# Optimization experiments

Hardware: AMD Instinct MI355X
Metric: run time of the kernel (lower is better)

## Reference

```python
import jax, jax.numpy as jnp
import numpy as np

S = 32        # num_subdomains
D = 1         # in_size
WIDTH = 128   # width_size
DEPTH = 4     # eqx MLP depth -> 1 input layer + (DEPTH-1) hidden layers + 1 output layer
N = 262144    # collocation points
TOL = 1e-8


def setup_inputs() -> dict:
    key = jax.random.key(0)
    ks = jax.random.split(key, 7)
    # subdomain i = [(i-0.5)/S, (i+1.5)/S] -> center (i+0.5)/S, half-width 1/S
    centers = ((jnp.arange(S, dtype=jnp.float32) + 0.5) / S)[:, None]          # (S, D)
    scales = jnp.full((S, D), 1.0 / S, dtype=jnp.float32)                       # (S, D)

    def unif(k, shape, fan_in):  # equinox Linear init: U(-1/sqrt(fan_in), 1/sqrt(fan_in))
        lim = 1.0 / np.sqrt(fan_in)
        return jax.random.uniform(k, shape, jnp.float32, -lim, lim)

    W_in = unif(ks[0], (S, WIDTH, D), D)
    b_in = unif(ks[1], (S, WIDTH), D)
    W_hid = unif(ks[2], (S, DEPTH - 1, WIDTH, WIDTH), WIDTH)
    b_hid = unif(ks[3], (S, DEPTH - 1, WIDTH), WIDTH)
    W_out = unif(ks[4], (S, 1, WIDTH), WIDTH)
    b_out = unif(ks[5], (S, 1), WIDTH)
    x = jax.random.uniform(ks[6], (N, D), jnp.float32, 0.0, 1.0)
    return {"x": x, "W_in": W_in, "b_in": b_in, "W_hid": W_hid, "b_hid": b_hid,
            "W_out": W_out, "b_out": b_out, "centers": centers, "scales": scales}


def reference(x, W_in, b_in, W_hid, b_hid, W_out, b_out, centers, scales):
    # normalized coords per subdomain: (S, n, D)
    u = (x[None, :, :] - centers[:, None, :]) / scales[:, None, :]
    # partition-of-unity cosine window, product over dims, normalized over subdomains
    raw = jnp.prod(jnp.where(jnp.abs(u) < 1.0, jnp.cos(0.5 * jnp.pi * u) ** 2, 0.0), axis=-1)  # (S, n)
    w = raw / (jnp.sum(raw, axis=0, keepdims=True) + TOL)                                       # (S, n)

    def body(total, p):
        Wi, bi, Wh, bh, Wo, bo, xn, wk = p
        h = jnp.tanh(xn @ Wi.T + bi)                      # (n, WIDTH)
        for l in range(DEPTH - 1):                        # static unroll over hidden layers
            h = jnp.tanh(h @ Wh[l].T + bh[l])
        out = (h @ Wo.T + bo)[:, 0]                       # (n,)
        return total + wk * out, None

    total, _ = jax.lax.scan(body, jnp.zeros(x.shape[0], x.dtype),
                            (W_in, b_in, W_hid, b_hid, W_out, b_out, u, w))
    # ansatz = identity
    return total
```

## Files before the change

### kernel.cpp

```cpp
#include <hip/hip_runtime.h>

#define NS 32
#define WID 128
#define NHID 3
#define NPTS 262144
#define PTILE 256
#define TMLP 512
#define TPB 68

#define TASKS_OFF 512
#define WF_OFF (TASKS_OFF + 2 * NPTS * 4)
#define TANH_C 2.8853900817779268f

typedef _Float16 f16x2 __attribute__((ext_vector_type(2)));
typedef _Float16 f16x4 __attribute__((ext_vector_type(4)));
typedef _Float16 f16x8 __attribute__((ext_vector_type(8)));
typedef __fp16 fp16x2 __attribute__((ext_vector_type(2)));
typedef float f32x4 __attribute__((ext_vector_type(4)));

union U4H8 { uint4 u; f16x8 h; };
union PK2 { fp16x2 p; f16x2 h; };

__device__ __forceinline__ f16x2 pk2(float a, float b) {
    PK2 u; u.p = __builtin_amdgcn_cvt_pkrtz(a, b); return u.h;
}

__device__ __forceinline__ float tanh_fast(float v) {
    float a = v * TANH_C;
    float e; asm("v_exp_f32 %0, %1" : "=v"(e) : "v"(a));
    float d = e + 1.0f;
    float r; asm("v_rcp_f32 %0, %1" : "=v"(r) : "v"(d));
    return fmaf(-2.0f, r, 1.0f);
}

__device__ __forceinline__ float tanh_pre(float a) {
    float e; asm("v_exp_f32 %0, %1" : "=v"(e) : "v"(a));
    float d = e + 1.0f;
    float r; asm("v_rcp_f32 %0, %1" : "=v"(r) : "v"(d));
    return fmaf(-2.0f, r, 1.0f);
}

__device__ __forceinline__ float coswin(float u) {
    if (fabsf(u) >= 1.0f) return 0.0f;
    float rev = u * 0.25f;
    float c; asm("v_cos_f32 %0, %1" : "=v"(c) : "v"(rev));
    return c * c;
}


__global__ void k_count(const float* __restrict__ x, int* __restrict__ counts, int n) {
    __shared__ int loc[NS];
    int t = threadIdx.x;
    if (t < NS) loc[t] = 0;
    __syncthreads();
    int i = blockIdx.x * blockDim.x + t;
    if (i < n) {
        float tt = x[i] * 32.0f;
        int j = (int)floorf(tt); j = min(max(j, 0), 31);
        atomicAdd(&loc[j], 1);
        float u = tt - (float)j - 0.5f;
        int nb = (u > 0.0f) ? j + 1 : j - 1;
        if (u != 0.0f && nb >= 0 && nb < NS) atomicAdd(&loc[nb], 1);
    }
    __syncthreads();
    if (t < NS) atomicAdd(&counts[t], loc[t]);
}

__global__ void k_scan(const int* __restrict__ counts, int* __restrict__ offsets,
                       int* __restrict__ cursors) {
    if (threadIdx.x == 0) {
        int acc = 0;
        for (int s = 0; s < NS; ++s) { offsets[s] = acc; cursors[s] = acc; acc += counts[s]; }
    }
}

__global__ void k_scatter(const float* __restrict__ x, int* __restrict__ cursors,
                          int* __restrict__ tasks, int n) {
    __shared__ int loc[NS];
    __shared__ int base[NS];
    int t = threadIdx.x;
    if (t < NS) loc[t] = 0;
    __syncthreads();
    int i = blockIdx.x * blockDim.x + t;
    int j = -1, nb = -1, sj = 0, snb = 0;
    if (i < n) {
        float tt = x[i] * 32.0f;
        j = min(max((int)floorf(tt), 0), 31);
        sj = atomicAdd(&loc[j], 1);
        float u = tt - (float)j - 0.5f;
        int nb2 = (u > 0.0f) ? j + 1 : j - 1;
        if (u != 0.0f && nb2 >= 0 && nb2 < NS) { nb = nb2; snb = atomicAdd(&loc[nb], 1); }
    }
    __syncthreads();
    if (t < NS) base[t] = atomicAdd(&cursors[t], loc[t]);
    __syncthreads();
    if (i < n) {
        tasks[base[j] + sj] = i;
        if (nb >= 0) tasks[base[nb] + snb] = i;
    }
}


__global__ void k_prepw(const float* __restrict__ Wh, uint4* __restrict__ WfU4) {
    int tid = blockIdx.x * blockDim.x + threadIdx.x;
    if (tid >= 32 * 3 * 8 * 4 * 64) return;
    int lane = tid & 63;
    int s    = (tid >> 6) & 3;
    int t8   = (tid >> 8) & 7;
    int v    = tid >> 11;
    int o    = 16 * t8 + (lane & 15);
    const float* src = Wh + ((size_t)v * 128 + o) * 128;
    unsigned short b[8];
#pragma unroll
    for (int e = 0; e < 8; ++e) {
        int k = 32 * s + 4 * (lane >> 4) + (e & 3) + 16 * (e >> 2);
        _Float16 hv = (_Float16)(src[k] * TANH_C);
        b[e] = *(unsigned short*)&hv;
    }
    uint4 outv;
    outv.x = (unsigned)b[0] | ((unsigned)b[1] << 16);
    outv.y = (unsigned)b[2] | ((unsigned)b[3] << 16);
    outv.z = (unsigned)b[4] | ((unsigned)b[5] << 16);
    outv.w = (unsigned)b[6] | ((unsigned)b[7] << 16);
    WfU4[((size_t)(v * 8 + t8) * 4 + s) * 64 + lane] = outv;
}


__global__ __launch_bounds__(TMLP, 4) void k_mlp(
    const float* __restrict__ x, const float* __restrict__ W_in, const float* __restrict__ b_in,
    const float* __restrict__ b_hid, const float* __restrict__ W_out, const float* __restrict__ b_out,
    const float* __restrict__ centers, const float* __restrict__ scales,
    const int* __restrict__ counts, const int* __restrict__ offsets, const int* __restrict__ tasks,
    const uint4* __restrict__ WfU4, float* __restrict__ out) {

    const int bin = blockIdx.y;
    const int tile = blockIdx.x;
    const int cnt = counts[bin];
    if (tile * PTILE >= cnt) return;
    const int start = offsets[bin];

    __shared__ __align__(256) _Float16 HT[8][4096];
    __shared__ float lU[PTILE], lWgt[PTILE];
    __shared__ int lTid[PTILE];

    const int t = threadIdx.x;
    const int lane = t & 63;
    const int l15 = t & 15;
    const int g = (t >> 4) & 3;
    const int w = t >> 6;

    if (t < PTILE) {
        int idx = tile * PTILE + t;
        if (idx < cnt) {
            int pid = tasks[start + idx];
            lTid[t] = pid;
            float xx = x[pid];
            float u = (xx - centers[bin]) * (1.0f / scales[bin]);
            lU[t] = u;
            float rs = coswin(u);
            int other = bin + (u > 0.0f ? 1 : -1);
            float ro = 0.0f;
            if (other >= 0 && other < NS)
                ro = coswin((xx - centers[other]) * (1.0f / scales[other]));
            lWgt[t] = rs / (rs + ro + 1e-8f);
        } else { lTid[t] = -1; lU[t] = 0.0f; lWgt[t] = 0.0f; }
    }
    __syncthreads();

    {
        float4 ua = *(const float4*)&lU[w * 32 + 4 * g];
        float4 ub = *(const float4*)&lU[w * 32 + 16 + 4 * g];
        const float* Win = W_in + bin * WID;
        const float* Bi  = b_in + bin * WID;
#pragma unroll
        for (int t8 = 0; t8 < 8; ++t8) {
            int o = 16 * t8 + l15;
            float wv = Win[o], bv = Bi[o];
            f16x2 h00 = pk2(tanh_fast(fmaf(ua.x, wv, bv)), tanh_fast(fmaf(ua.y, wv, bv)));
            f16x2 h01 = pk2(tanh_fast(fmaf(ua.z, wv, bv)), tanh_fast(fmaf(ua.w, wv, bv)));
            f16x2 h10 = pk2(tanh_fast(fmaf(ub.x, wv, bv)), tanh_fast(fmaf(ub.y, wv, bv)));
            f16x2 h11 = pk2(tanh_fast(fmaf(ub.z, wv, bv)), tanh_fast(fmaf(ub.w, wv, bv)));
            *(f16x4*)&HT[w][o * 16 + 4 * g] = __builtin_shufflevector(h00, h01, 0, 1, 2, 3);
            *(f16x4*)&HT[w][2048 + o * 16 + 4 * g] = __builtin_shufflevector(h10, h11, 0, 1, 2, 3);
        }
    }

    const unsigned htaddr = (unsigned)(size_t)&HT[w][0] + lane * 8;
    const uint4* wfbase = WfU4 + (size_t)(bin * NHID) * 32 * 64 + lane;
    float p0 = 0.f, p1 = 0.f, p2 = 0.f, p3 = 0.f;
    float q0 = 0.f, q1 = 0.f, q2 = 0.f, q3 = 0.f;

#pragma unroll
    for (int lyr = 0; lyr < NHID; ++lyr) {
        f16x4 r0, r1, r2, r3, r4, r5, r6, r7, r8, r9, r10, r11, r12, r13, r14, r15;
        asm volatile(
            "ds_read_b64_tr_b16 %0, %16 offset:0\n\t"
            "ds_read_b64_tr_b16 %1, %16 offset:512\n\t"
            "ds_read_b64_tr_b16 %2, %16 offset:1024\n\t"
            "ds_read_b64_tr_b16 %3, %16 offset:1536\n\t"
            "ds_read_b64_tr_b16 %4, %16 offset:2048\n\t"
            "ds_read_b64_tr_b16 %5, %16 offset:2560\n\t"
            "ds_read_b64_tr_b16 %6, %16 offset:3072\n\t"
            "ds_read_b64_tr_b16 %7, %16 offset:3584\n\t"
            "ds_read_b64_tr_b16 %8, %16 offset:4096\n\t"
            "ds_read_b64_tr_b16 %9, %16 offset:4608\n\t"
            "ds_read_b64_tr_b16 %10, %16 offset:5120\n\t"
            "ds_read_b64_tr_b16 %11, %16 offset:5632\n\t"
            "ds_read_b64_tr_b16 %12, %16 offset:6144\n\t"
            "ds_read_b64_tr_b16 %13, %16 offset:6656\n\t"
            "ds_read_b64_tr_b16 %14, %16 offset:7168\n\t"
            "ds_read_b64_tr_b16 %15, %16 offset:7680\n\t"
            "s_waitcnt lgkmcnt(0)"
            : "=v"(r0), "=v"(r1), "=v"(r2), "=v"(r3), "=v"(r4), "=v"(r5), "=v"(r6), "=v"(r7),
              "=v"(r8), "=v"(r9), "=v"(r10), "=v"(r11), "=v"(r12), "=v"(r13), "=v"(r14), "=v"(r15)
            : "v"(htaddr) : "memory");
        f16x8 A0[4], A1[4];
        A0[0] = __builtin_shufflevector(r0, r1, 0, 1, 2, 3, 4, 5, 6, 7);
        A0[1] = __builtin_shufflevector(r2, r3, 0, 1, 2, 3, 4, 5, 6, 7);
        A0[2] = __builtin_shufflevector(r4, r5, 0, 1, 2, 3, 4, 5, 6, 7);
        A0[3] = __builtin_shufflevector(r6, r7, 0, 1, 2, 3, 4, 5, 6, 7);
        A1[0] = __builtin_shufflevector(r8, r9, 0, 1, 2, 3, 4, 5, 6, 7);
        A1[1] = __builtin_shufflevector(r10, r11, 0, 1, 2, 3, 4, 5, 6, 7);
        A1[2] = __builtin_shufflevector(r12, r13, 0, 1, 2, 3, 4, 5, 6, 7);
        A1[3] = __builtin_shufflevector(r14, r15, 0, 1, 2, 3, 4, 5, 6, 7);

        const float* bh = b_hid + (size_t)(bin * NHID + lyr) * WID;
        float bhv[8];
#pragma unroll
        for (int t8 = 0; t8 < 8; ++t8) bhv[t8] = bh[16 * t8 + l15] * TANH_C;

        const uint4* wfL = wfbase + (size_t)lyr * 32 * 64;

        uint4 cur[4], nxt[4];
#pragma unroll
        for (int s = 0; s < 4; ++s) cur[s] = wfL[s * 64];

#pragma unroll
        for (int t8 = 0; t8 < 8; ++t8) {
            if (t8 < 7) {
#pragma unroll
                for (int s = 0; s < 4; ++s) nxt[s] = wfL[((t8 + 1) * 4 + s) * 64];
            }
            f32x4 acc0 = (f32x4){0.f, 0.f, 0.f, 0.f};
            f32x4 acc1 = (f32x4){0.f, 0.f, 0.f, 0.f};
            __builtin_amdgcn_s_setprio(1);
#pragma unroll
            for (int s = 0; s < 4; ++s) {
                U4H8 bw; bw.u = cur[s];
                acc0 = __builtin_amdgcn_mfma_f32_16x16x32_f16(A0[s], bw.h, acc0, 0, 0, 0);
                acc1 = __builtin_amdgcn_mfma_f32_16x16x32_f16(A1[s], bw.h, acc1, 0, 0, 0);
            }
            __builtin_amdgcn_s_setprio(0);

            if (lyr < NHID - 1) {
                int o = 16 * t8 + l15;
                float bv = bhv[t8];
                f16x2 h00 = pk2(tanh_pre(acc0[0] + bv), tanh_pre(acc0[1] + bv));
                f16x2 h01 = pk2(tanh_pre(acc0[2] + bv), tanh_pre(acc0[3] + bv));
                f16x2 h10 = pk2(tanh_pre(acc1[0] + bv), tanh_pre(acc1[1] + bv));
                f16x2 h11 = pk2(tanh_pre(acc1[2] + bv), tanh_pre(acc1[3] + bv));
                *(f16x4*)&HT[w][o * 16 + 4 * g] = __builtin_shufflevector(h00, h01, 0, 1, 2, 3);
                *(f16x4*)&HT[w][2048 + o * 16 + 4 * g] = __builtin_shufflevector(h10, h11, 0, 1, 2, 3);
            } else {
                float bv = bhv[t8];
                float wv = W_out[bin * WID + 16 * t8 + l15];
                p0 = fmaf(wv, tanh_pre(acc0[0] + bv), p0);
                p1 = fmaf(wv, tanh_pre(acc0[1] + bv), p1);
                p2 = fmaf(wv, tanh_pre(acc0[2] + bv), p2);
                p3 = fmaf(wv, tanh_pre(acc0[3] + bv), p3);
                q0 = fmaf(wv, tanh_pre(acc1[0] + bv), q0);
                q1 = fmaf(wv, tanh_pre(acc1[1] + bv), q1);
                q2 = fmaf(wv, tanh_pre(acc1[2] + bv), q2);
                q3 = fmaf(wv, tanh_pre(acc1[3] + bv), q3);
            }
#pragma unroll
            for (int s = 0; s < 4; ++s) cur[s] = nxt[s];
        }
    }

#pragma unroll
    for (int m = 1; m < 16; m <<= 1) {
        p0 += __shfl_xor(p0, m); p1 += __shfl_xor(p1, m);
        p2 += __shfl_xor(p2, m); p3 += __shfl_xor(p3, m);
        q0 += __shfl_xor(q0, m); q1 += __shfl_xor(q1, m);
        q2 += __shfl_xor(q2, m); q3 += __shfl_xor(q3, m);
    }
    if (l15 < 4) {
        float bo = b_out[bin];
        float v0 = ((l15 == 0) ? p0 : (l15 == 1) ? p1 : (l15 == 2) ? p2 : p3) + bo;
        float v1 = ((l15 == 0) ? q0 : (l15 == 1) ? q1 : (l15 == 2) ? q2 : q3) + bo;
        int pl0 = w * 32 + 4 * g + l15;
        int pl1 = pl0 + 16;
        int pid0 = lTid[pl0], pid1 = lTid[pl1];
        if (pid0 >= 0) atomicAdd(out + pid0, lWgt[pl0] * v0);
        if (pid1 >= 0) atomicAdd(out + pid1, lWgt[pl1] * v1);
    }
}

extern "C" void kernel_launch(void* const* d_in, const int* in_sizes, int n_in,
                              void* d_out, int out_size, void* d_ws, size_t ws_size,
                              hipStream_t stream) {
    const float* x       = (const float*)d_in[0];
    const float* W_in    = (const float*)d_in[1];
    const float* b_in    = (const float*)d_in[2];
    const float* W_hid   = (const float*)d_in[3];
    const float* b_hid   = (const float*)d_in[4];
    const float* W_out   = (const float*)d_in[5];
    const float* b_out   = (const float*)d_in[6];
    const float* centers = (const float*)d_in[7];
    const float* scales  = (const float*)d_in[8];
    float* out = (float*)d_out;

    char* ws = (char*)d_ws;
    int* counts  = (int*)(ws);
    int* cursors = (int*)(ws + 128);
    int* offsets = (int*)(ws + 256);
    int* tasks   = (int*)(ws + TASKS_OFF);
    uint4* WfU4  = (uint4*)(ws + WF_OFF);

    (void)hipMemsetAsync(d_out, 0, (size_t)out_size * sizeof(float), stream);
    (void)hipMemsetAsync(ws, 0, 256, stream);

    k_prepw<<<dim3(768), dim3(256), 0, stream>>>(W_hid, WfU4);
    k_count<<<dim3(NPTS / 256), dim3(256), 0, stream>>>(x, counts, NPTS);
    k_scan<<<1, 32, 0, stream>>>(counts, offsets, cursors);
    k_scatter<<<dim3(NPTS / 256), dim3(256), 0, stream>>>(x, cursors, tasks, NPTS);
    k_mlp<<<dim3(TPB, NS), dim3(TMLP), 0, stream>>>(x, W_in, b_in, b_hid, W_out, b_out,
                                                    centers, scales, counts, offsets, tasks,
                                                    WfU4, out);
}
```

Measured before the change: 135.0 us.

## Use fixed-capacity bins, fuse output zeroing, double-buffer MLP weight prefetch

Replaces the count, scan and scatter sequence with a single scatter kernel. It writes each point's task into a fixed-capacity slot per subdomain and also zeroes the output, which removes two kernel launches and a memset. In the MLP kernel the weight fragments are loaded through two alternating buffers, with the first fragment of the next layer prefetched early, and bias and output weights are hoisted to the start of each layer. The fixed bin capacity assumes no subdomain receives more than CAP points, which holds for roughly uniform inputs but would overflow for skewed ones.

```diff
diff --git a/kernel.cpp b/kernel.cpp
--- a/kernel.cpp
+++ b/kernel.cpp
@@ -6,10 +6,11 @@
 #define NPTS 262144
 #define PTILE 256
 #define TMLP 512
-#define TPB 68
+#define CAP 17408
+#define TPB (CAP / PTILE)
 
 #define TASKS_OFF 512
-#define WF_OFF (TASKS_OFF + 2 * NPTS * 4)
+#define WF_OFF (TASKS_OFF + NS * CAP * 4)
 #define TANH_C 2.8853900817779268f
 
 typedef _Float16 f16x2 __attribute__((ext_vector_type(2)));
@@ -48,34 +49,8 @@
 }
 
 
-__global__ void k_count(const float* __restrict__ x, int* __restrict__ counts, int n) {
-    __shared__ int loc[NS];
-    int t = threadIdx.x;
-    if (t < NS) loc[t] = 0;
-    __syncthreads();
-    int i = blockIdx.x * blockDim.x + t;
-    if (i < n) {
-        float tt = x[i] * 32.0f;
-        int j = (int)floorf(tt); j = min(max(j, 0), 31);
-        atomicAdd(&loc[j], 1);
-        float u = tt - (float)j - 0.5f;
-        int nb = (u > 0.0f) ? j + 1 : j - 1;
-        if (u != 0.0f && nb >= 0 && nb < NS) atomicAdd(&loc[nb], 1);
-    }
-    __syncthreads();
-    if (t < NS) atomicAdd(&counts[t], loc[t]);
-}
-
-__global__ void k_scan(const int* __restrict__ counts, int* __restrict__ offsets,
-                       int* __restrict__ cursors) {
-    if (threadIdx.x == 0) {
-        int acc = 0;
-        for (int s = 0; s < NS; ++s) { offsets[s] = acc; cursors[s] = acc; acc += counts[s]; }
-    }
-}
-
-__global__ void k_scatter(const float* __restrict__ x, int* __restrict__ cursors,
-                          int* __restrict__ tasks, int n) {
+__global__ void k_scatter2(const float* __restrict__ x, int* __restrict__ cursors,
+                           int* __restrict__ tasks, float* __restrict__ out, int n) {
     __shared__ int loc[NS];
     __shared__ int base[NS];
     int t = threadIdx.x;
@@ -84,6 +59,7 @@
     int i = blockIdx.x * blockDim.x + t;
     int j = -1, nb = -1, sj = 0, snb = 0;
     if (i < n) {
+        out[i] = 0.0f;
         float tt = x[i] * 32.0f;
         j = min(max((int)floorf(tt), 0), 31);
         sj = atomicAdd(&loc[j], 1);
@@ -95,8 +71,8 @@
     if (t < NS) base[t] = atomicAdd(&cursors[t], loc[t]);
     __syncthreads();
     if (i < n) {
-        tasks[base[j] + sj] = i;
-        if (nb >= 0) tasks[base[nb] + snb] = i;
+        tasks[j * CAP + base[j] + sj] = i;
+        if (nb >= 0) tasks[nb * CAP + base[nb] + snb] = i;
     }
 }
 
@@ -130,14 +106,14 @@
     const float* __restrict__ x, const float* __restrict__ W_in, const float* __restrict__ b_in,
     const float* __restrict__ b_hid, const float* __restrict__ W_out, const float* __restrict__ b_out,
     const float* __restrict__ centers, const float* __restrict__ scales,
-    const int* __restrict__ counts, const int* __restrict__ offsets, const int* __restrict__ tasks,
+    const int* __restrict__ cursors, const int* __restrict__ tasks,
     const uint4* __restrict__ WfU4, float* __restrict__ out) {
 
     const int bin = blockIdx.y;
     const int tile = blockIdx.x;
-    const int cnt = counts[bin];
+    const int cnt = cursors[bin];
     if (tile * PTILE >= cnt) return;
-    const int start = offsets[bin];
+    const int start = bin * CAP;
 
     __shared__ __align__(256) _Float16 HT[8][4096];
     __shared__ float lU[PTILE], lWgt[PTILE];
@@ -167,6 +143,12 @@
     }
     __syncthreads();
 
+    const uint4* wfbase = WfU4 + (size_t)(bin * NHID) * 32 * 64 + lane;
+
+    uint4 bufA[4], bufB[4];
+#pragma unroll
+    for (int s = 0; s < 4; ++s) bufA[s] = wfbase[s * 64];
+
     {
         float4 ua = *(const float4*)&lU[w * 32 + 4 * g];
         float4 ub = *(const float4*)&lU[w * 32 + 16 + 4 * g];
@@ -186,12 +168,20 @@
     }
 
     const unsigned htaddr = (unsigned)(size_t)&HT[w][0] + lane * 8;
-    const uint4* wfbase = WfU4 + (size_t)(bin * NHID) * 32 * 64 + lane;
     float p0 = 0.f, p1 = 0.f, p2 = 0.f, p3 = 0.f;
     float q0 = 0.f, q1 = 0.f, q2 = 0.f, q3 = 0.f;
 
 #pragma unroll
     for (int lyr = 0; lyr < NHID; ++lyr) {
+        const float* bh = b_hid + (size_t)(bin * NHID + lyr) * WID;
+        float bhv[8], wov[8];
+#pragma unroll
+        for (int t8 = 0; t8 < 8; ++t8) bhv[t8] = bh[16 * t8 + l15] * TANH_C;
+        if (lyr == NHID - 1) {
+#pragma unroll
+            for (int t8 = 0; t8 < 8; ++t8) wov[t8] = W_out[bin * WID + 16 * t8 + l15];
+        }
+
         f16x4 r0, r1, r2, r3, r4, r5, r6, r7, r8, r9, r10, r11, r12, r13, r14, r15;
         asm volatile(
             "ds_read_b64_tr_b16 %0, %16 offset:0\n\t"
@@ -224,37 +214,29 @@
         A1[2] = __builtin_shufflevector(r12, r13, 0, 1, 2, 3, 4, 5, 6, 7);
         A1[3] = __builtin_shufflevector(r14, r15, 0, 1, 2, 3, 4, 5, 6, 7);
 
-        const float* bh = b_hid + (size_t)(bin * NHID + lyr) * WID;
-        float bhv[8];
-#pragma unroll
-        for (int t8 = 0; t8 < 8; ++t8) bhv[t8] = bh[16 * t8 + l15] * TANH_C;
-
         const uint4* wfL = wfbase + (size_t)lyr * 32 * 64;
-
-        uint4 cur[4], nxt[4];
-#pragma unroll
-        for (int s = 0; s < 4; ++s) cur[s] = wfL[s * 64];
-
-#pragma unroll
-        for (int t8 = 0; t8 < 8; ++t8) {
-            if (t8 < 7) {
-#pragma unroll
-                for (int s = 0; s < 4; ++s) nxt[s] = wfL[((t8 + 1) * 4 + s) * 64];
-            }
+        const uint4* wfN = wfbase + (size_t)(lyr + 1) * 32 * 64;
+
+#pragma unroll
+        for (int tp = 0; tp < 4; ++tp) {
+            const int t8a = 2 * tp, t8b = 2 * tp + 1;
+#pragma unroll
+            for (int s = 0; s < 4; ++s) bufB[s] = wfL[(t8b * 4 + s) * 64];
+
             f32x4 acc0 = (f32x4){0.f, 0.f, 0.f, 0.f};
             f32x4 acc1 = (f32x4){0.f, 0.f, 0.f, 0.f};
             __builtin_amdgcn_s_setprio(1);
 #pragma unroll
             for (int s = 0; s < 4; ++s) {
-                U4H8 bw; bw.u = cur[s];
+                U4H8 bw; bw.u = bufA[s];
                 acc0 = __builtin_amdgcn_mfma_f32_16x16x32_f16(A0[s], bw.h, acc0, 0, 0, 0);
                 acc1 = __builtin_amdgcn_mfma_f32_16x16x32_f16(A1[s], bw.h, acc1, 0, 0, 0);
             }
             __builtin_amdgcn_s_setprio(0);
 
             if (lyr < NHID - 1) {
-                int o = 16 * t8 + l15;
-                float bv = bhv[t8];
+                int o = 16 * t8a + l15;
+                float bv = bhv[t8a];
                 f16x2 h00 = pk2(tanh_pre(acc0[0] + bv), tanh_pre(acc0[1] + bv));
                 f16x2 h01 = pk2(tanh_pre(acc0[2] + bv), tanh_pre(acc0[3] + bv));
                 f16x2 h10 = pk2(tanh_pre(acc1[0] + bv), tanh_pre(acc1[1] + bv));
@@ -262,8 +244,7 @@
                 *(f16x4*)&HT[w][o * 16 + 4 * g] = __builtin_shufflevector(h00, h01, 0, 1, 2, 3);
                 *(f16x4*)&HT[w][2048 + o * 16 + 4 * g] = __builtin_shufflevector(h10, h11, 0, 1, 2, 3);
             } else {
-                float bv = bhv[t8];
-                float wv = W_out[bin * WID + 16 * t8 + l15];
+                float bv = bhv[t8a], wv = wov[t8a];
                 p0 = fmaf(wv, tanh_pre(acc0[0] + bv), p0);
                 p1 = fmaf(wv, tanh_pre(acc0[1] + bv), p1);
                 p2 = fmaf(wv, tanh_pre(acc0[2] + bv), p2);
@@ -273,8 +254,46 @@
                 q2 = fmaf(wv, tanh_pre(acc1[2] + bv), q2);
                 q3 = fmaf(wv, tanh_pre(acc1[3] + bv), q3);
             }
-#pragma unroll
-            for (int s = 0; s < 4; ++s) cur[s] = nxt[s];
+
+            if (t8b < 7) {
+#pragma unroll
+                for (int s = 0; s < 4; ++s) bufA[s] = wfL[((t8b + 1) * 4 + s) * 64];
+            } else if (lyr < NHID - 1) {
+#pragma unroll
+                for (int s = 0; s < 4; ++s) bufA[s] = wfN[s * 64];
+            }
+
+            f32x4 bcc0 = (f32x4){0.f, 0.f, 0.f, 0.f};
+            f32x4 bcc1 = (f32x4){0.f, 0.f, 0.f, 0.f};
+            __builtin_amdgcn_s_setprio(1);
+#pragma unroll
+            for (int s = 0; s < 4; ++s) {
+                U4H8 bw; bw.u = bufB[s];
+                bcc0 = __builtin_amdgcn_mfma_f32_16x16x32_f16(A0[s], bw.h, bcc0, 0, 0, 0);
+                bcc1 = __builtin_amdgcn_mfma_f32_16x16x32_f16(A1[s], bw.h, bcc1, 0, 0, 0);
+            }
+            __builtin_amdgcn_s_setprio(0);
+
+            if (lyr < NHID - 1) {
+                int o = 16 * t8b + l15;
+                float bv = bhv[t8b];
+                f16x2 h00 = pk2(tanh_pre(bcc0[0] + bv), tanh_pre(bcc0[1] + bv));
+                f16x2 h01 = pk2(tanh_pre(bcc0[2] + bv), tanh_pre(bcc0[3] + bv));
+                f16x2 h10 = pk2(tanh_pre(bcc1[0] + bv), tanh_pre(bcc1[1] + bv));
+                f16x2 h11 = pk2(tanh_pre(bcc1[2] + bv), tanh_pre(bcc1[3] + bv));
+                *(f16x4*)&HT[w][o * 16 + 4 * g] = __builtin_shufflevector(h00, h01, 0, 1, 2, 3);
+                *(f16x4*)&HT[w][2048 + o * 16 + 4 * g] = __builtin_shufflevector(h10, h11, 0, 1, 2, 3);
+            } else {
+                float bv = bhv[t8b], wv = wov[t8b];
+                p0 = fmaf(wv, tanh_pre(bcc0[0] + bv), p0);
+                p1 = fmaf(wv, tanh_pre(bcc0[1] + bv), p1);
+                p2 = fmaf(wv, tanh_pre(bcc0[2] + bv), p2);
+                p3 = fmaf(wv, tanh_pre(bcc0[3] + bv), p3);
+                q0 = fmaf(wv, tanh_pre(bcc1[0] + bv), q0);
+                q1 = fmaf(wv, tanh_pre(bcc1[1] + bv), q1);
+                q2 = fmaf(wv, tanh_pre(bcc1[2] + bv), q2);
+                q3 = fmaf(wv, tanh_pre(bcc1[3] + bv), q3);
+            }
         }
     }
 
@@ -312,20 +331,15 @@
     float* out = (float*)d_out;
 
     char* ws = (char*)d_ws;
-    int* counts  = (int*)(ws);
-    int* cursors = (int*)(ws + 128);
-    int* offsets = (int*)(ws + 256);
+    int* cursors = (int*)(ws);
     int* tasks   = (int*)(ws + TASKS_OFF);
     uint4* WfU4  = (uint4*)(ws + WF_OFF);
 
-    (void)hipMemsetAsync(d_out, 0, (size_t)out_size * sizeof(float), stream);
     (void)hipMemsetAsync(ws, 0, 256, stream);
 
     k_prepw<<<dim3(768), dim3(256), 0, stream>>>(W_hid, WfU4);
-    k_count<<<dim3(NPTS / 256), dim3(256), 0, stream>>>(x, counts, NPTS);
-    k_scan<<<1, 32, 0, stream>>>(counts, offsets, cursors);
-    k_scatter<<<dim3(NPTS / 256), dim3(256), 0, stream>>>(x, cursors, tasks, NPTS);
+    k_scatter2<<<dim3(NPTS / 256), dim3(256), 0, stream>>>(x, cursors, tasks, out, NPTS);
     k_mlp<<<dim3(TPB, NS), dim3(TMLP), 0, stream>>>(x, W_in, b_in, b_hid, W_out, b_out,
-                                                    centers, scales, counts, offsets, tasks,
+                                                    centers, scales, cursors, tasks,
                                                     WfU4, out);
 }
```

Result: faster. 117.0 us (-13.3%).
